# Performance work log

Measured on AMD Instinct MI355X. Metric: run time of the kernel, lower is better.

## Reference

```python
import jax, jax.numpy as jnp
import numpy as np

D_MODEL = 1024
N_HEADS = 16
HEAD_DIM = D_MODEL // N_HEADS


def setup_inputs() -> dict:
    key = jax.random.key(0)
    ks = jax.random.split(key, 5)
    x = jax.random.normal(ks[0], (4, 2048, D_MODEL), dtype=jnp.float32)
    # qkv Linear: weight [3*d_model, d_model], bias [3*d_model]
    w_qkv = jax.random.normal(ks[1], (3 * D_MODEL, D_MODEL), dtype=jnp.float32) / np.sqrt(D_MODEL)
    b_qkv = jnp.zeros((3 * D_MODEL,), dtype=jnp.float32)
    w_out = jax.random.normal(ks[2], (D_MODEL, D_MODEL), dtype=jnp.float32) / np.sqrt(D_MODEL)
    b_out = jnp.zeros((D_MODEL,), dtype=jnp.float32)
    return {"x": x, "w_qkv": w_qkv, "b_qkv": b_qkv, "w_out": w_out, "b_out": b_out}


def reference(x, w_qkv, b_qkv, w_out, b_out):
    B, T, C = x.shape
    H, Dh = N_HEADS, HEAD_DIM
    qkv = x @ w_qkv.T + b_qkv                      # [B,T,3C]
    qkv = qkv.reshape(B, T, 3, H, Dh)
    q = jnp.transpose(qkv[:, :, 0], (0, 2, 1, 3))  # [B,H,T,Dh]
    k = jnp.transpose(qkv[:, :, 1], (0, 2, 1, 3))
    v = jnpp_transpose = jnp.transpose(qkv[:, :, 2], (0, 2, 1, 3))
    scale = 1.0 / np.sqrt(Dh).astype(np.float32)
    att = jnp.einsum('bhqd,bhkd->bhqk', q, k) * scale
    causal = jnp.tril(jnp.ones((T, T), dtype=bool))
    att = jnp.where(causal[None, None], att, -jnp.inf)
    att = jax.nn.softmax(att, axis=-1)
    head_out = jnp.einsum('bhqk,bhkd->bhqd', att, v)  # [B,H,T,Dh]
    out = jnp.transpose(head_out, (0, 2, 1, 3)).reshape(B, T, C)
    return out @ w_out.T + b_out
```

## Files before the change

kernel.cpp:

```cpp
#include <hip/hip_runtime.h>
#include <hip/hip_bf16.h>


#define D_MODEL 1024
#define N_HEADS 16
#define HEAD_DIM 64
#define SEQ 2048
#define BATCH 4

#define NX (BATCH * SEQ * D_MODEL)
#define NWQ (3 * D_MODEL * D_MODEL)
#define NWO (D_MODEL * D_MODEL)

typedef __attribute__((ext_vector_type(8))) short bf16x8;
typedef __attribute__((ext_vector_type(4))) float f32x4;
typedef unsigned int uint;

__device__ __forceinline__ short f2bf(float f) {
    union { float f; uint i; } c; c.f = f;
    uint x = c.i;
    x += 0x7fffu + ((x >> 16) & 1u);
    return (short)(x >> 16);
}
__device__ __forceinline__ uint pack2(float a, float b) {
    return (uint)(unsigned short)f2bf(a) | ((uint)(unsigned short)f2bf(b) << 16);
}
__device__ __forceinline__ uint asu(float f) { union { float f; uint i; } c; c.f = f; return c.i; }
__device__ __forceinline__ uint packtr(float lo, float hi) {
    return (asu(lo) >> 16) | (asu(hi) & 0xffff0000u);
}

__device__ __forceinline__ void glds16(const void* g, void* l) {
    __builtin_amdgcn_global_load_lds(
        (const __attribute__((address_space(1))) uint*)g,
        (__attribute__((address_space(3))) uint*)l, 16, 0, 0);
}

__global__ __launch_bounds__(256) void cvt_all(const float* __restrict__ x,
                                               const float* __restrict__ wq,
                                               const float* __restrict__ wo,
                                               short* __restrict__ dst) {
    int i = (blockIdx.x * 256 + threadIdx.x) * 4;
    const float* src; int off;
    if (i < NX)            { src = x;  off = 0; }
    else if (i < NX + NWQ) { src = wq; off = NX; }
    else                   { src = wo; off = NX + NWQ; }
    float4 f = *(const float4*)(src + (i - off));
    uint2 o; o.x = pack2(f.x, f.y); o.y = pack2(f.z, f.w);
    *(uint2*)(dst + i) = o;
}

template <int MODE>
__global__ __launch_bounds__(256, 2) void gemm_bt(
    const short* __restrict__ A, const short* __restrict__ B,
    const float* __restrict__ bias, float* __restrict__ Cp,
    int M, int N, int K,
    short* __restrict__ qp, short* __restrict__ kp, short* __restrict__ vp)
{
    __shared__ short As[128][32];
    __shared__ short Bs[128][32];
    const int tid = threadIdx.x;
    const int wave = tid >> 6, lane = tid & 63;
    const int quad = lane >> 4, l16 = lane & 15;
    const int wm = (wave >> 1) * 64, wn = (wave & 1) * 64;
    const int rowBase = blockIdx.y * 128;
    const int colBase = blockIdx.x * 128;

    const short* gA = A + (size_t)(rowBase + wave * 32 + (lane >> 2)) * K + (lane & 3) * 8;
    const short* gB = B + (size_t)(colBase + wave * 32 + (lane >> 2)) * K + (lane & 3) * 8;
    void* lA0 = &As[wave * 32][0];
    void* lA1 = &As[wave * 32 + 16][0];
    void* lB0 = &Bs[wave * 32][0];
    void* lB1 = &Bs[wave * 32 + 16][0];

    f32x4 acc[4][4] = {};

    for (int k0 = 0; k0 < K; k0 += 32) {
        __syncthreads();
        glds16(gA + k0, lA0);
        glds16(gA + (size_t)16 * K + k0, lA1);
        glds16(gB + k0, lB0);
        glds16(gB + (size_t)16 * K + k0, lB1);
        __syncthreads();
        bf16x8 af[4], bfr[4];
#pragma unroll
        for (int i = 0; i < 4; ++i)
            af[i] = *(const bf16x8*)&As[wm + i * 16 + l16][quad * 8];
#pragma unroll
        for (int j = 0; j < 4; ++j)
            bfr[j] = *(const bf16x8*)&Bs[wn + j * 16 + l16][quad * 8];
#pragma unroll
        for (int i = 0; i < 4; ++i)
#pragma unroll
            for (int j = 0; j < 4; ++j)
                acc[i][j] = __builtin_amdgcn_mfma_f32_16x16x32_bf16(bfr[j], af[i], acc[i][j], 0, 0, 0);
    }

#pragma unroll
    for (int i = 0; i < 4; ++i) {
#pragma unroll
        for (int j = 0; j < 4; ++j) {
            const int row = rowBase + wm + i * 16 + l16;
            const int col = colBase + wn + j * 16 + quad * 4;
            float4 bv = *(const float4*)&bias[col];
            float v0 = acc[i][j][0] + bv.x;
            float v1 = acc[i][j][1] + bv.y;
            float v2 = acc[i][j][2] + bv.z;
            float v3 = acc[i][j][3] + bv.w;
            if (MODE == 0) {
                float4 o = {v0, v1, v2, v3};
                *(float4*)&Cp[(size_t)row * N + col] = o;
            } else {
                int which = col >> 10;
                int h = (col >> 6) & 15;
                int d = col & 63;
                int b = row >> 11;
                int t = row & 2047;
                short* dst = (which == 0) ? qp : (which == 1) ? kp : vp;
                uint2 u; u.x = pack2(v0, v1); u.y = pack2(v2, v3);
                *(uint2*)&dst[((((size_t)b * N_HEADS + h) * SEQ) + t) * HEAD_DIM + d] = u;
            }
        }
    }
}

__global__ __launch_bounds__(256, 2) void attn_fwd(
    const short* __restrict__ Q, const short* __restrict__ K,
    const short* __restrict__ V, short* __restrict__ O)
{
    __shared__ short Ks[64][72];
    __shared__ short Vt[80][72];
    __shared__ short Ps[128][72];
    const int tid = threadIdx.x;
    const int wave = tid >> 6, lane = tid & 63;
    const int quad = lane >> 4, l16 = lane & 15;
    const int bh = blockIdx.x;
    const int b = bh >> 4, h = bh & 15;
    const int qt = gridDim.y - 1 - blockIdx.y;
    const int qbase = qt * 128;
    const short* Qh = Q + (size_t)bh * SEQ * HEAD_DIM;
    const short* Kh = K + (size_t)bh * SEQ * HEAD_DIM;
    const short* Vh = V + (size_t)bh * SEQ * HEAD_DIM;

    for (int idx = tid; idx < 16 * 72; idx += 256)
        Vt[64 + idx / 72][idx % 72] = (idx < 72) ? (short)0x3F80 : (short)0;

    bf16x8 qf[2][2];
#pragma unroll
    for (int m = 0; m < 2; ++m)
#pragma unroll
        for (int st = 0; st < 2; ++st)
            qf[m][st] = *(const bf16x8*)(Qh + (size_t)(qbase + wave * 32 + m * 16 + l16) * HEAD_DIM + st * 32 + quad * 8);

    f32x4 o[2][4] = {};
    f32x4 o4[2] = {};
    const float C1 = 0.125f * 1.44269504f;
    const float C2 = 14.4269504f;

    const int kr = tid >> 2, kc = (tid & 3) * 16;
    const int vk = (tid & 31) * 2, vd = (tid >> 5) * 8;
    const int subw = qbase + wave * 32;

    const int ntiles = 2 * qt + 2;
    int4 kv0 = *(const int4*)(Kh + (size_t)kr * HEAD_DIM + kc);
    int4 kv1 = *(const int4*)(Kh + (size_t)kr * HEAD_DIM + kc + 8);
    int4 vv0 = *(const int4*)(Vh + (size_t)vk * HEAD_DIM + vd);
    int4 vv1 = *(const int4*)(Vh + (size_t)(vk + 1) * HEAD_DIM + vd);

    for (int j = 0; j < ntiles; ++j) {
        const int kb = j * 64;
        __syncthreads();
        *(int4*)&Ks[kr][kc] = kv0;
        *(int4*)&Ks[kr][kc + 8] = kv1;
        {
            const short* va = (const short*)&vv0;
            const short* vb = (const short*)&vv1;
#pragma unroll
            for (int e = 0; e < 8; ++e)
                *(uint*)&Vt[vd + e][vk] =
                    (uint)(unsigned short)va[e] | ((uint)(unsigned short)vb[e] << 16);
        }
        __syncthreads();

        {
            const int kbn = (j + 1 < ntiles) ? kb + 64 : kb;
            kv0 = *(const int4*)(Kh + (size_t)(kbn + kr) * HEAD_DIM + kc);
            kv1 = *(const int4*)(Kh + (size_t)(kbn + kr) * HEAD_DIM + kc + 8);
            vv0 = *(const int4*)(Vh + (size_t)(kbn + vk) * HEAD_DIM + vd);
            vv1 = *(const int4*)(Vh + (size_t)(kbn + vk + 1) * HEAD_DIM + vd);
        }

        if (kb > subw + 31) continue;

        f32x4 s[2][4];
#pragma unroll
        for (int kt = 0; kt < 4; ++kt) {
            bf16x8 kf0 = *(const bf16x8*)&Ks[kt * 16 + l16][quad * 8];
            bf16x8 kf1 = *(const bf16x8*)&Ks[kt * 16 + l16][32 + quad * 8];
#pragma unroll
            for (int m = 0; m < 2; ++m) {
                f32x4 t = {0.f, 0.f, 0.f, 0.f};
                t = __builtin_amdgcn_mfma_f32_16x16x32_bf16(kf0, qf[m][0], t, 0, 0, 0);
                t = __builtin_amdgcn_mfma_f32_16x16x32_bf16(kf1, qf[m][1], t, 0, 0, 0);
                s[m][kt] = t;
            }
        }
#pragma unroll
        for (int m = 0; m < 2; ++m) {
            const int sub = subw + m * 16;
            const int qrow = sub + l16;
            const bool needmask = (kb + 63 > sub);
            const int prow = wave * 32 + m * 16 + l16;
#pragma unroll
            for (int kt = 0; kt < 4; ++kt) {
                float p[4];
#pragma unroll
                for (int r = 0; r < 4; ++r) {
                    float a = __builtin_fmaf(s[m][kt][r], C1, -C2);
                    if (needmask && (kb + kt * 16 + quad * 4 + r > qrow)) a = -1e30f;
                    p[r] = __builtin_exp2f(a);
                }
                uint2 u; u.x = packtr(p[0], p[1]); u.y = packtr(p[2], p[3]);
                *(uint2*)&Ps[prow][kt * 16 + quad * 4] = u;
            }
        }
#pragma unroll
        for (int st = 0; st < 2; ++st) {
            bf16x8 pf0 = *(const bf16x8*)&Ps[wave * 32 + l16][st * 32 + quad * 8];
            bf16x8 pf1 = *(const bf16x8*)&Ps[wave * 32 + 16 + l16][st * 32 + quad * 8];
            bf16x8 vf4 = *(const bf16x8*)&Vt[64 + l16][st * 32 + quad * 8];
#pragma unroll
            for (int dt = 0; dt < 4; ++dt) {
                bf16x8 vf = *(const bf16x8*)&Vt[dt * 16 + l16][st * 32 + quad * 8];
                o[0][dt] = __builtin_amdgcn_mfma_f32_16x16x32_bf16(pf0, vf, o[0][dt], 0, 0, 0);
                o[1][dt] = __builtin_amdgcn_mfma_f32_16x16x32_bf16(pf1, vf, o[1][dt], 0, 0, 0);
            }
            o4[0] = __builtin_amdgcn_mfma_f32_16x16x32_bf16(pf0, vf4, o4[0], 0, 0, 0);
            o4[1] = __builtin_amdgcn_mfma_f32_16x16x32_bf16(pf1, vf4, o4[1], 0, 0, 0);
        }
    }

#pragma unroll
    for (int m = 0; m < 2; ++m) {
#pragma unroll
        for (int r = 0; r < 4; ++r) {
            float lq = __shfl(o4[m][r], quad << 4);
            float inv = 1.f / lq;
            int t = qbase + wave * 32 + m * 16 + quad * 4 + r;
            size_t base = ((size_t)b * SEQ + t) * D_MODEL + h * HEAD_DIM;
#pragma unroll
            for (int dt = 0; dt < 4; ++dt)
                O[base + dt * 16 + l16] = f2bf(o[m][dt][r] * inv);
        }
    }
}

extern "C" void kernel_launch(void* const* d_in, const int* in_sizes, int n_in,
                              void* d_out, int out_size, void* d_ws, size_t ws_size,
                              hipStream_t stream)
{
    const float* x     = (const float*)d_in[0];
    const float* w_qkv = (const float*)d_in[1];
    const float* b_qkv = (const float*)d_in[2];
    const float* w_out = (const float*)d_in[3];
    const float* b_out = (const float*)d_in[4];
    float* out = (float*)d_out;

    const size_t HE = (size_t)BATCH * N_HEADS * SEQ * HEAD_DIM;

    short* xb    = (short*)d_ws;
    short* wqkvb = xb + NX;
    short* woutb = wqkvb + NWQ;
    short* qp    = woutb + NWO;
    short* kp    = qp + HE;
    short* vp    = kp + HE;
    short* ho    = xb;

    const int M = BATCH * SEQ;

    cvt_all<<<(NX + NWQ + NWO) / 1024, 256, 0, stream>>>(x, w_qkv, w_out, xb);

    gemm_bt<1><<<dim3(3 * D_MODEL / 128, M / 128), 256, 0, stream>>>(
        xb, wqkvb, b_qkv, nullptr, M, 3 * D_MODEL, D_MODEL, qp, kp, vp);

    attn_fwd<<<dim3(BATCH * N_HEADS, SEQ / 128), 256, 0, stream>>>(qp, kp, vp, ho);

    gemm_bt<0><<<dim3(D_MODEL / 128, M / 128), 256, 0, stream>>>(
        ho, woutb, b_out, out, M, D_MODEL, D_MODEL, nullptr, nullptr, nullptr);
}
```

Baseline: 264.2 us.

## Pair causal query tiles per block, fold softmax scale into Q, sum rowsums in registers

The attention kernel now handles two query tiles per block (tile 15-y and tile y), so every block does the same amount of causal work, and the grid is halved. The softmax scale and log2e are folded into Q inside the QKV GEMM epilogue, and the constant offset goes into the MFMA accumulator init, which removes the per-element FMA. The row sum is now accumulated in registers and reduced with shuffles, replacing the extra ones-column MFMA and its LDS rows. The GEMM launch bounds also rise to 3 blocks per CU, which may limit registers. Halving the grid to 512 blocks reduces parallelism on a GPU with many CUs.

```diff
diff --git a/kernel.cpp b/kernel.cpp
--- a/kernel.cpp
+++ b/kernel.cpp
@@ -50,8 +50,9 @@
     *(uint2*)(dst + i) = o;
 }
 
+#define QSCALE 0.18033688f
 template <int MODE>
-__global__ __launch_bounds__(256, 2) void gemm_bt(
+__global__ __launch_bounds__(256, 3) void gemm_bt(
     const short* __restrict__ A, const short* __restrict__ B,
     const float* __restrict__ bias, float* __restrict__ Cp,
     int M, int N, int K,
@@ -112,6 +113,7 @@
                 *(float4*)&Cp[(size_t)row * N + col] = o;
             } else {
                 int which = col >> 10;
+                if (which == 0) { v0 *= QSCALE; v1 *= QSCALE; v2 *= QSCALE; v3 *= QSCALE; }
                 int h = (col >> 6) & 15;
                 int d = col & 63;
                 int b = row >> 11;
@@ -129,128 +131,131 @@
     const short* __restrict__ V, short* __restrict__ O)
 {
     __shared__ short Ks[64][72];
-    __shared__ short Vt[80][72];
+    __shared__ short Vt[64][72];
     __shared__ short Ps[128][72];
     const int tid = threadIdx.x;
     const int wave = tid >> 6, lane = tid & 63;
     const int quad = lane >> 4, l16 = lane & 15;
     const int bh = blockIdx.x;
     const int b = bh >> 4, h = bh & 15;
-    const int qt = gridDim.y - 1 - blockIdx.y;
-    const int qbase = qt * 128;
     const short* Qh = Q + (size_t)bh * SEQ * HEAD_DIM;
     const short* Kh = K + (size_t)bh * SEQ * HEAD_DIM;
     const short* Vh = V + (size_t)bh * SEQ * HEAD_DIM;
 
-    for (int idx = tid; idx < 16 * 72; idx += 256)
-        Vt[64 + idx / 72][idx % 72] = (idx < 72) ? (short)0x3F80 : (short)0;
-
-    bf16x8 qf[2][2];
-#pragma unroll
-    for (int m = 0; m < 2; ++m)
-#pragma unroll
-        for (int st = 0; st < 2; ++st)
-            qf[m][st] = *(const bf16x8*)(Qh + (size_t)(qbase + wave * 32 + m * 16 + l16) * HEAD_DIM + st * 32 + quad * 8);
-
-    f32x4 o[2][4] = {};
-    f32x4 o4[2] = {};
-    const float C1 = 0.125f * 1.44269504f;
-    const float C2 = 14.4269504f;
+    const float NC2 = -14.4269504f;
 
     const int kr = tid >> 2, kc = (tid & 3) * 16;
     const int vk = (tid & 31) * 2, vd = (tid >> 5) * 8;
-    const int subw = qbase + wave * 32;
-
-    const int ntiles = 2 * qt + 2;
-    int4 kv0 = *(const int4*)(Kh + (size_t)kr * HEAD_DIM + kc);
-    int4 kv1 = *(const int4*)(Kh + (size_t)kr * HEAD_DIM + kc + 8);
-    int4 vv0 = *(const int4*)(Vh + (size_t)vk * HEAD_DIM + vd);
-    int4 vv1 = *(const int4*)(Vh + (size_t)(vk + 1) * HEAD_DIM + vd);
-
-    for (int j = 0; j < ntiles; ++j) {
-        const int kb = j * 64;
-        __syncthreads();
-        *(int4*)&Ks[kr][kc] = kv0;
-        *(int4*)&Ks[kr][kc + 8] = kv1;
-        {
-            const short* va = (const short*)&vv0;
-            const short* vb = (const short*)&vv1;
-#pragma unroll
-            for (int e = 0; e < 8; ++e)
-                *(uint*)&Vt[vd + e][vk] =
-                    (uint)(unsigned short)va[e] | ((uint)(unsigned short)vb[e] << 16);
+
+#pragma unroll
+    for (int phase = 0; phase < 2; ++phase) {
+        const int qt = phase ? blockIdx.y : (15 - blockIdx.y);
+        const int qbase = qt * 128;
+        const int subw = qbase + wave * 32;
+        const int ntiles = 2 * qt + 2;
+
+        bf16x8 qf[2][2];
+#pragma unroll
+        for (int m = 0; m < 2; ++m)
+#pragma unroll
+            for (int st = 0; st < 2; ++st)
+                qf[m][st] = *(const bf16x8*)(Qh + (size_t)(qbase + wave * 32 + m * 16 + l16) * HEAD_DIM + st * 32 + quad * 8);
+
+        f32x4 o[2][4] = {};
+        f32x4 lsum4[2] = {};
+
+        int4 kv0 = *(const int4*)(Kh + (size_t)kr * HEAD_DIM + kc);
+        int4 kv1 = *(const int4*)(Kh + (size_t)kr * HEAD_DIM + kc + 8);
+        int4 vv0 = *(const int4*)(Vh + (size_t)vk * HEAD_DIM + vd);
+        int4 vv1 = *(const int4*)(Vh + (size_t)(vk + 1) * HEAD_DIM + vd);
+
+        for (int j = 0; j < ntiles; ++j) {
+            const int kb = j * 64;
+            __syncthreads();
+            *(int4*)&Ks[kr][kc] = kv0;
+            *(int4*)&Ks[kr][kc + 8] = kv1;
+            {
+                const short* va = (const short*)&vv0;
+                const short* vb = (const short*)&vv1;
+#pragma unroll
+                for (int e = 0; e < 8; ++e)
+                    *(uint*)&Vt[vd + e][vk] =
+                        (uint)(unsigned short)va[e] | ((uint)(unsigned short)vb[e] << 16);
+            }
+            __syncthreads();
+
+            {
+                const int kbn = (j + 1 < ntiles) ? kb + 64 : kb;
+                kv0 = *(const int4*)(Kh + (size_t)(kbn + kr) * HEAD_DIM + kc);
+                kv1 = *(const int4*)(Kh + (size_t)(kbn + kr) * HEAD_DIM + kc + 8);
+                vv0 = *(const int4*)(Vh + (size_t)(kbn + vk) * HEAD_DIM + vd);
+                vv1 = *(const int4*)(Vh + (size_t)(kbn + vk + 1) * HEAD_DIM + vd);
+            }
+
+            if (kb > subw + 31) continue;
+
+            f32x4 s[2][4];
+#pragma unroll
+            for (int kt = 0; kt < 4; ++kt) {
+                bf16x8 kf0 = *(const bf16x8*)&Ks[kt * 16 + l16][quad * 8];
+                bf16x8 kf1 = *(const bf16x8*)&Ks[kt * 16 + l16][32 + quad * 8];
+#pragma unroll
+                for (int m = 0; m < 2; ++m) {
+                    f32x4 t = {NC2, NC2, NC2, NC2};
+                    t = __builtin_amdgcn_mfma_f32_16x16x32_bf16(kf0, qf[m][0], t, 0, 0, 0);
+                    t = __builtin_amdgcn_mfma_f32_16x16x32_bf16(kf1, qf[m][1], t, 0, 0, 0);
+                    s[m][kt] = t;
+                }
+            }
+#pragma unroll
+            for (int m = 0; m < 2; ++m) {
+                const int sub = subw + m * 16;
+                const int qrow = sub + l16;
+                const bool needmask = (kb + 63 > sub);
+                const int prow = wave * 32 + m * 16 + l16;
+#pragma unroll
+                for (int kt = 0; kt < 4; ++kt) {
+                    float p[4];
+#pragma unroll
+                    for (int r = 0; r < 4; ++r) {
+                        float a = s[m][kt][r];
+                        if (needmask && (kb + kt * 16 + quad * 4 + r > qrow)) a = -1e30f;
+                        p[r] = __builtin_exp2f(a);
+                    }
+                    lsum4[m] += (f32x4){p[0], p[1], p[2], p[3]};
+                    uint2 u; u.x = packtr(p[0], p[1]); u.y = packtr(p[2], p[3]);
+                    *(uint2*)&Ps[prow][kt * 16 + quad * 4] = u;
+                }
+            }
+#pragma unroll
+            for (int st = 0; st < 2; ++st) {
+                bf16x8 pf0 = *(const bf16x8*)&Ps[wave * 32 + l16][st * 32 + quad * 8];
+                bf16x8 pf1 = *(const bf16x8*)&Ps[wave * 32 + 16 + l16][st * 32 + quad * 8];
+#pragma unroll
+                for (int dt = 0; dt < 4; ++dt) {
+                    bf16x8 vf = *(const bf16x8*)&Vt[dt * 16 + l16][st * 32 + quad * 8];
+                    o[0][dt] = __builtin_amdgcn_mfma_f32_16x16x32_bf16(pf0, vf, o[0][dt], 0, 0, 0);
+                    o[1][dt] = __builtin_amdgcn_mfma_f32_16x16x32_bf16(pf1, vf, o[1][dt], 0, 0, 0);
+                }
+            }
         }
-        __syncthreads();
-
-        {
-            const int kbn = (j + 1 < ntiles) ? kb + 64 : kb;
-            kv0 = *(const int4*)(Kh + (size_t)(kbn + kr) * HEAD_DIM + kc);
-            kv1 = *(const int4*)(Kh + (size_t)(kbn + kr) * HEAD_DIM + kc + 8);
-            vv0 = *(const int4*)(Vh + (size_t)(kbn + vk) * HEAD_DIM + vd);
-            vv1 = *(const int4*)(Vh + (size_t)(kbn + vk + 1) * HEAD_DIM + vd);
-        }
-
-        if (kb > subw + 31) continue;
-
-        f32x4 s[2][4];
-#pragma unroll
-        for (int kt = 0; kt < 4; ++kt) {
-            bf16x8 kf0 = *(const bf16x8*)&Ks[kt * 16 + l16][quad * 8];
-            bf16x8 kf1 = *(const bf16x8*)&Ks[kt * 16 + l16][32 + quad * 8];
-#pragma unroll
-            for (int m = 0; m < 2; ++m) {
-                f32x4 t = {0.f, 0.f, 0.f, 0.f};
-                t = __builtin_amdgcn_mfma_f32_16x16x32_bf16(kf0, qf[m][0], t, 0, 0, 0);
-                t = __builtin_amdgcn_mfma_f32_16x16x32_bf16(kf1, qf[m][1], t, 0, 0, 0);
-                s[m][kt] = t;
-            }
-        }
+
 #pragma unroll
         for (int m = 0; m < 2; ++m) {
-            const int sub = subw + m * 16;
-            const int qrow = sub + l16;
-            const bool needmask = (kb + 63 > sub);
-            const int prow = wave * 32 + m * 16 + l16;
-#pragma unroll
-            for (int kt = 0; kt < 4; ++kt) {
-                float p[4];
-#pragma unroll
-                for (int r = 0; r < 4; ++r) {
-                    float a = __builtin_fmaf(s[m][kt][r], C1, -C2);
-                    if (needmask && (kb + kt * 16 + quad * 4 + r > qrow)) a = -1e30f;
-                    p[r] = __builtin_exp2f(a);
-                }
-                uint2 u; u.x = packtr(p[0], p[1]); u.y = packtr(p[2], p[3]);
-                *(uint2*)&Ps[prow][kt * 16 + quad * 4] = u;
-            }
-        }
-#pragma unroll
-        for (int st = 0; st < 2; ++st) {
-            bf16x8 pf0 = *(const bf16x8*)&Ps[wave * 32 + l16][st * 32 + quad * 8];
-            bf16x8 pf1 = *(const bf16x8*)&Ps[wave * 32 + 16 + l16][st * 32 + quad * 8];
-            bf16x8 vf4 = *(const bf16x8*)&Vt[64 + l16][st * 32 + quad * 8];
-#pragma unroll
-            for (int dt = 0; dt < 4; ++dt) {
-                bf16x8 vf = *(const bf16x8*)&Vt[dt * 16 + l16][st * 32 + quad * 8];
-                o[0][dt] = __builtin_amdgcn_mfma_f32_16x16x32_bf16(pf0, vf, o[0][dt], 0, 0, 0);
-                o[1][dt] = __builtin_amdgcn_mfma_f32_16x16x32_bf16(pf1, vf, o[1][dt], 0, 0, 0);
-            }
-            o4[0] = __builtin_amdgcn_mfma_f32_16x16x32_bf16(pf0, vf4, o4[0], 0, 0, 0);
-            o4[1] = __builtin_amdgcn_mfma_f32_16x16x32_bf16(pf1, vf4, o4[1], 0, 0, 0);
-        }
-    }
-
-#pragma unroll
-    for (int m = 0; m < 2; ++m) {
-#pragma unroll
-        for (int r = 0; r < 4; ++r) {
-            float lq = __shfl(o4[m][r], quad << 4);
-            float inv = 1.f / lq;
-            int t = qbase + wave * 32 + m * 16 + quad * 4 + r;
-            size_t base = ((size_t)b * SEQ + t) * D_MODEL + h * HEAD_DIM;
-#pragma unroll
-            for (int dt = 0; dt < 4; ++dt)
-                O[base + dt * 16 + l16] = f2bf(o[m][dt][r] * inv);
+            float l = lsum4[m][0] + lsum4[m][1] + lsum4[m][2] + lsum4[m][3];
+            l += __shfl_xor(l, 16);
+            l += __shfl_xor(l, 32);
+#pragma unroll
+            for (int r = 0; r < 4; ++r) {
+                int qloc = quad * 4 + r;
+                float lq = __shfl(l, qloc);
+                float inv = 1.f / lq;
+                int t = qbase + wave * 32 + m * 16 + qloc;
+                size_t base = ((size_t)b * SEQ + t) * D_MODEL + h * HEAD_DIM;
+#pragma unroll
+                for (int dt = 0; dt < 4; ++dt)
+                    O[base + dt * 16 + l16] = f2bf(o[m][dt][r] * inv);
+            }
         }
     }
 }
@@ -283,7 +288,7 @@
     gemm_bt<1><<<dim3(3 * D_MODEL / 128, M / 128), 256, 0, stream>>>(
         xb, wqkvb, b_qkv, nullptr, M, 3 * D_MODEL, D_MODEL, qp, kp, vp);
 
-    attn_fwd<<<dim3(BATCH * N_HEADS, SEQ / 128), 256, 0, stream>>>(qp, kp, vp, ho);
+    attn_fwd<<<dim3(BATCH * N_HEADS, SEQ / 256), 256, 0, stream>>>(qp, kp, vp, ho);
 
     gemm_bt<0><<<dim3(D_MODEL / 128, M / 128), 256, 0, stream>>>(
         ho, woutb, b_out, out, M, D_MODEL, D_MODEL, nullptr, nullptr, nullptr);
```

Result: slower. 272.9 us (+3.3%).
